# Optimization experiments

Measured on AMD Instinct MI355X. Metric: run time of the kernel, lower is better.

The kernel has to match this reference:

```python
import jax, jax.numpy as jnp
import numpy as np
import math

EMBED_DIM = 64

def setup_inputs() -> dict:
    key = jax.random.key(0)
    ks = jax.random.split(key, 9)
    B, S, H, E = 2, 2048, 8, EMBED_DIM
    f16 = jnp.float16
    inp = {
        'query': jax.random.normal(ks[0], (B, S, H, E), dtype=f16),
        'key':   jax.random.normal(ks[1], (B, S, H, E), dtype=f16),
        'value': jax.random.normal(ks[2], (B, S, H, E), dtype=f16),
        # Linear params (torch Linear: y = x @ W.T + b); W stored as [out,in]
        'Wq': (jax.random.normal(ks[3], (E, E), dtype=f16) / np.float16(math.sqrt(E))),
        'bq': jax.random.normal(ks[4], (E,), dtype=f16) * np.float16(0.02),
        'Wk': (jax.random.normal(ks[5], (E, E), dtype=f16) / np.float16(math.sqrt(E))),
        'bk': jax.random.normal(ks[6], (E,), dtype=f16) * np.float16(0.02),
        'Wv': (jax.random.normal(ks[7], (E, E), dtype=f16) / np.float16(math.sqrt(E))),
        'bv': jax.random.normal(ks[8], (E,), dtype=f16) * np.float16(0.02),
    }
    return inp

def reference(query, key, value, Wq, bq, Wk, bk, Wv, bv):
    # Linear projections on last dim, fused with permute(0,2,1,3): [B,S,H,E] -> [B,H,S,E]
    q = jnp.einsum('bshe,fe->bhsf', query, Wq) + bq
    k = jnp.einsum('bshe,fe->bhsf', key, Wk) + bk
    v = jnp.einsum('bshe,fe->bhsf', value, Wv) + bv
    scale = jnp.asarray(1.0 / math.sqrt(q.shape[-1]), dtype=q.dtype)
    q = q * scale
    # full attention matrix [B,H,S,S], fp16 matmul then fp32 softmax (faithful to source)
    scores = jnp.einsum('bhse,bhte->bhst', q, k).astype(jnp.float32)
    attn = jax.nn.softmax(scores, axis=-1).astype(jnp.float16)
    out = jnp.einsum('bhst,bhte->bhse', attn, v)
    return out
```

## Files before the change

### kernel.cpp

```cpp
#include <hip/hip_runtime.h>

#define S_LEN 2048
#define NH    8
#define EMB   64
#define BM    64
#define BN    64
#define NKT   (S_LEN / BN)
#define NSPLIT 2
#define M_INIT  (-1.0e4f)
#define EXP_CLAMP (-80.0f)
#define DEFER_THR 8.0f

typedef _Float16 half8   __attribute__((ext_vector_type(8)));
typedef _Float16 half4   __attribute__((ext_vector_type(4)));
typedef float    float4_t __attribute__((ext_vector_type(4)));
typedef float    float8_t __attribute__((ext_vector_type(8)));

__device__ inline half8 cvt8(const float* p) {
    float8_t f = *reinterpret_cast<const float8_t*>(p);
    half8 h;
    #pragma unroll
    for (int j = 0; j < 8; ++j) h[j] = (_Float16)f[j];
    return h;
}

__device__ inline void gload_lds16(const _Float16* g, _Float16* l) {
    __builtin_amdgcn_global_load_lds(
        (const __attribute__((address_space(1))) void*)g,
        (__attribute__((address_space(3))) void*)l, 16, 0, 0);
}

__device__ inline void proj_body(
    int mode, int bid, const float* __restrict__ X,
    const float* __restrict__ W, const float* __restrict__ bias,
    _Float16* __restrict__ Dst)
{
    const int tid  = threadIdx.x;
    const int lane = tid & 63;
    const int wave = tid >> 6;
    const int l15  = lane & 15;
    const int quad = lane >> 4;
    const int gwave = bid * 4 + wave;

    half8 wf[4][2];
    #pragma unroll
    for (int ft = 0; ft < 4; ++ft)
        #pragma unroll
        for (int ks = 0; ks < 2; ++ks)
            wf[ft][ks] = cvt8(W + (ft * 16 + l15) * 64 + ks * 32 + quad * 8);
    float bv[4];
    #pragma unroll
    for (int ft = 0; ft < 4; ++ft) bv[ft] = bias[ft * 16 + l15];

    #pragma unroll
    for (int rt2 = 0; rt2 < 2; ++rt2) {
        const int rt = gwave * 2 + rt2;
        const int arow = rt * 16 + l15;
        half8 xf[2];
        #pragma unroll
        for (int ks = 0; ks < 2; ++ks)
            xf[ks] = cvt8(X + (long)arow * 64 + ks * 32 + quad * 8);
        float4_t acc[4];
        #pragma unroll
        for (int ft = 0; ft < 4; ++ft) {
            acc[ft] = (float4_t){0.f, 0.f, 0.f, 0.f};
            #pragma unroll
            for (int ks = 0; ks < 2; ++ks)
                acc[ft] = __builtin_amdgcn_mfma_f32_16x16x32_f16(
                    xf[ks], wf[ft][ks], acc[ft], 0, 0, 0);
        }
        #pragma unroll
        for (int r = 0; r < 4; ++r) {
            const int row = rt * 16 + quad * 4 + r;
            const int b = row >> 14;
            const int s = (row >> 3) & 2047;
            const int h = row & 7;
            const int bh = b * NH + h;
            #pragma unroll
            for (int ft = 0; ft < 4; ++ft) {
                const _Float16 v = (_Float16)(acc[ft][r] + bv[ft]);
                const int f = ft * 16 + l15;
                if (mode == 0)
                    Dst[((long)bh * S_LEN + s) * EMB + f] = v * (_Float16)0.125f;
                else if (mode == 1)
                    Dst[(((long)bh * 8 + (f >> 3)) * S_LEN + s) * 8 + (f & 7)] = v;
                else
                    Dst[(((long)bh * 256 + (s >> 3)) * 64 + f) * 8 + (s & 7)] = v;
            }
        }
    }
}

__global__ __launch_bounds__(256) void proj_qk(
    const float* __restrict__ q_in, const float* __restrict__ k_in,
    const float* __restrict__ Wq, const float* __restrict__ bq,
    const float* __restrict__ Wk, const float* __restrict__ bk,
    _Float16* __restrict__ Qf16, _Float16* __restrict__ KT8)
{
    const int seg = blockIdx.x >> 8;
    const int bid = blockIdx.x & 255;
    if (seg == 0) proj_body(0, bid, q_in, Wq, bq, Qf16);
    else          proj_body(1, bid, k_in, Wk, bk, KT8);
}

__global__ __launch_bounds__(256) void proj_v(
    const float* __restrict__ v_in,
    const float* __restrict__ Wv, const float* __restrict__ bv_,
    _Float16* __restrict__ VT8)
{
    proj_body(2, blockIdx.x, v_in, Wv, bv_, VT8);
}

__global__ __launch_bounds__(256, 4) void attn_part(
    const _Float16* __restrict__ KT, const _Float16* __restrict__ VT,
    const _Float16* __restrict__ Qf16,
    _Float16* __restrict__ p0, _Float16* __restrict__ p1,
    float* __restrict__ stats)
{
    __shared__ __align__(16) _Float16 Kb[2][8 * 64 * 8];
    __shared__ __align__(16) _Float16 Vb[2][8 * 64 * 8];
    __shared__ __align__(16) _Float16 Pl[4][16 * 64];

    const int tid  = threadIdx.x;
    const int lane = tid & 63;
    const int wave = tid >> 6;
    const int l15  = lane & 15;
    const int quad = lane >> 4;

    const int bx     = blockIdx.x;
    const int xcd    = bx & 7;
    const int j      = bx >> 3;
    const int hh     = j >> 6;
    const int within = j & 63;
    const int bh     = xcd * 2 + hh;
    const int qt     = within >> 1;
    const int sp     = within & 1;

    const int qrow0 = qt * BM + wave * 16;
    const _Float16* kg  = KT + (long)bh * 8 * S_LEN * 8;
    const _Float16* vgh = VT + (long)bh * 256 * 512;

    const _Float16* k0 = kg + ((long)(tid >> 6) * S_LEN + (tid & 63)) * 8;
    const _Float16* k1 = kg + ((long)((tid >> 6) + 4) * S_LEN + (tid & 63)) * 8;
    const _Float16* v0 = vgh + tid * 8;
    const _Float16* v1 = vgh + (256 + tid) * 8;

    const int kb = sp * (NKT / NSPLIT), ke = kb + (NKT / NSPLIT);

    {
        const long t8  = (long)(kb * BN) * 8;
        const long t64 = (long)(kb * BN) * 64;
        gload_lds16(k0 + t8,  &Kb[0][tid * 8]);
        gload_lds16(k1 + t8,  &Kb[0][(256 + tid) * 8]);
        gload_lds16(v0 + t64, &Vb[0][tid * 8]);
        gload_lds16(v1 + t64, &Vb[0][(256 + tid) * 8]);
    }

    half8 qf[2];
    {
        const _Float16* qrow = Qf16 + ((long)bh * S_LEN + qrow0 + l15) * EMB;
        qf[0] = *reinterpret_cast<const half8*>(qrow + quad * 8);
        qf[1] = *reinterpret_cast<const half8*>(qrow + 32 + quad * 8);
    }

    half8 vones;
    #pragma unroll
    for (int jj = 0; jj < 8; ++jj) vones[jj] = (_Float16)1.0f;

    float4_t o[4];
    #pragma unroll
    for (int et = 0; et < 4; ++et) o[et] = (float4_t){0.f, 0.f, 0.f, 0.f};
    float4_t lacc = (float4_t){0.f, 0.f, 0.f, 0.f};
    float m_run = M_INIT;

    const int pswz = (l15 & 7) << 3;
    _Float16* Pw = Pl[wave];

    __syncthreads();

    for (int kt = kb; kt < ke; ++kt) {
        const int cur = (kt - kb) & 1;
        const bool more = (kt + 1 < ke);

        if (more) {
            const long t8  = (long)((kt + 1) * BN) * 8;
            const long t64 = (long)((kt + 1) * BN) * 64;
            _Float16* kd = Kb[cur ^ 1];
            _Float16* vd = Vb[cur ^ 1];
            gload_lds16(k0 + t8,  kd + tid * 8);
            gload_lds16(k1 + t8,  kd + (256 + tid) * 8);
            gload_lds16(v0 + t64, vd + tid * 8);
            gload_lds16(v1 + t64, vd + (256 + tid) * 8);
        }

        const _Float16* Kc = Kb[cur];
        const _Float16* Vc = Vb[cur];

        float4_t sacc[4];
        #pragma unroll
        for (int nt = 0; nt < 4; ++nt) sacc[nt] = (float4_t){0.f, 0.f, 0.f, 0.f};
        __builtin_amdgcn_s_setprio(1);
        #pragma unroll
        for (int nt = 0; nt < 4; ++nt)
            #pragma unroll
            for (int ks = 0; ks < 2; ++ks) {
                half8 kf = *reinterpret_cast<const half8*>(
                    Kc + (ks * 4 + quad) * 512 + (nt * 16 + l15) * 8);
                sacc[nt] = __builtin_amdgcn_mfma_f32_16x16x32_f16(
                    kf, qf[ks], sacc[nt], 0, 0, 0);
            }
        __builtin_amdgcn_s_setprio(0);

        float mx = fmaxf(fmaxf(sacc[0][0], sacc[0][1]),
                         fmaxf(sacc[0][2], sacc[0][3]));
        mx = fmaxf(fmaxf(mx, sacc[1][0]), sacc[1][1]);
        mx = fmaxf(fmaxf(mx, sacc[1][2]), sacc[1][3]);
        mx = fmaxf(fmaxf(mx, sacc[2][0]), sacc[2][1]);
        mx = fmaxf(fmaxf(mx, sacc[2][2]), sacc[2][3]);
        mx = fmaxf(fmaxf(mx, sacc[3][0]), sacc[3][1]);
        mx = fmaxf(fmaxf(mx, sacc[3][2]), sacc[3][3]);

        if (!__all(mx - m_run <= DEFER_THR)) {
            float mr = fmaxf(mx, __shfl_xor(mx, 16));
            mr = fmaxf(mr, __shfl_xor(mr, 32));
            const float mn = fmaxf(m_run, mr);
            const float alpha = __expf(fmaxf(m_run - mn, EXP_CLAMP));
            m_run = mn;
            #pragma unroll
            for (int r = 0; r < 4; ++r) {
                const float ar = __shfl(alpha, quad * 4 + r);
                lacc[r] *= ar;
                #pragma unroll
                for (int et = 0; et < 4; ++et) o[et][r] *= ar;
            }
        }

        #pragma unroll
        for (int ts = 0; ts < 2; ++ts) {
            #pragma unroll
            for (int ntl = 0; ntl < 2; ++ntl) {
                const int nt = ts * 2 + ntl;
                half4 ph;
                #pragma unroll
                for (int r = 0; r < 4; ++r)
                    ph[r] = (_Float16)__expf(sacc[nt][r] - m_run);
                *reinterpret_cast<half4*>(
                    &Pw[l15 * 64 + ((nt * 16 + quad * 4) ^ pswz)]) = ph;
            }
            half8 pf = *reinterpret_cast<const half8*>(
                &Pw[l15 * 64 + ((ts * 32 + quad * 8) ^ pswz)]);
            __builtin_amdgcn_s_setprio(1);
            #pragma unroll
            for (int et = 0; et < 4; ++et) {
                half8 vf = *reinterpret_cast<const half8*>(
                    Vc + (ts * 4 + quad) * 512 + (et * 16 + l15) * 8);
                o[et] = __builtin_amdgcn_mfma_f32_16x16x32_f16(pf, vf, o[et], 0, 0, 0);
            }
            lacc = __builtin_amdgcn_mfma_f32_16x16x32_f16(pf, vones, lacc, 0, 0, 0);
            __builtin_amdgcn_s_setprio(0);
        }

        if (more) __syncthreads();
    }

    _Float16* pp = (sp == 0) ? p0 : p1;
    #pragma unroll
    for (int r = 0; r < 4; ++r) {
        const float inv = 1.f / lacc[r];
        const int row = qrow0 + quad * 4 + r;
        const int R = bh * S_LEN + row;
        #pragma unroll
        for (int et = 0; et < 4; ++et)
            pp[(long)R * EMB + et * 16 + l15] = (_Float16)(o[et][r] * inv);
    }
    {
        const int srcl = (lane >> 2) * 16;
        const float s0 = __shfl(lacc[0], srcl);
        const float s1 = __shfl(lacc[1], srcl);
        const float s2 = __shfl(lacc[2], srcl);
        const float s3 = __shfl(lacc[3], srcl);
        const int rr = lane & 3;
        const float lsel = (rr == 0) ? s0 : (rr == 1) ? s1 : (rr == 2) ? s2 : s3;
        if (lane < 16) {
            const int R = bh * S_LEN + qrow0 + lane;
            stats[sp * 32768 + R] = m_run;
            stats[(NSPLIT + sp) * 32768 + R] = lsel;
        }
    }
}

__global__ __launch_bounds__(256) void attn_combine(
    const _Float16* __restrict__ p0, const _Float16* __restrict__ p1,
    const float* __restrict__ stats, float* __restrict__ out)
{
    const int gid = blockIdx.x * 256 + threadIdx.x;
    const int R  = gid >> 2;
    const int c0 = (gid & 3) * 16;
    const float m0 = stats[R], m1 = stats[32768 + R];
    const float l0 = stats[2 * 32768 + R], l1 = stats[3 * 32768 + R];
    const float M = fmaxf(m0, m1);
    float w0 = l0 * __expf(fmaxf(m0 - M, EXP_CLAMP));
    float w1 = l1 * __expf(fmaxf(m1 - M, EXP_CLAMP));
    const float rinv = 1.f / (w0 + w1);
    w0 *= rinv; w1 *= rinv;
    const long i0 = (long)R * EMB + c0;
    #pragma unroll
    for (int h = 0; h < 2; ++h) {
        half8 a = *reinterpret_cast<const half8*>(p0 + i0 + h * 8);
        half8 b = *reinterpret_cast<const half8*>(p1 + i0 + h * 8);
        #pragma unroll
        for (int j = 0; j < 8; ++j)
            out[i0 + h * 8 + j] = (float)(_Float16)(
                w0 * (float)a[j] + w1 * (float)b[j]);
    }
}

extern "C" void kernel_launch(void* const* d_in, const int* in_sizes, int n_in,
                              void* d_out, int out_size, void* d_ws, size_t ws_size,
                              hipStream_t stream) {
    const float* q_in = (const float*)d_in[0];
    const float* k_in = (const float*)d_in[1];
    const float* v_in = (const float*)d_in[2];
    const float* Wq   = (const float*)d_in[3];
    const float* bq   = (const float*)d_in[4];
    const float* Wk   = (const float*)d_in[5];
    const float* bk   = (const float*)d_in[6];
    const float* Wv   = (const float*)d_in[7];
    const float* bv   = (const float*)d_in[8];
    float* out = (float*)d_out;

    _Float16* Qf16  = (_Float16*)d_out;
    _Float16* KT8   = (_Float16*)((char*)d_out + (4u << 20));
    _Float16* VT8   = (_Float16*)d_in[1];
    _Float16* part0 = (_Float16*)d_in[2];
    _Float16* part1 = part0 + (long)2 * 1024 * 1024;
    float*    stats = (float*)d_in[0];

    proj_qk<<<512, 256, 0, stream>>>(q_in, k_in, Wq, bq, Wk, bk, Qf16, KT8);
    proj_v<<<256, 256, 0, stream>>>(v_in, Wv, bv, VT8);
    attn_part<<<16 * 32 * NSPLIT, 256, 0, stream>>>(KT8, VT8, Qf16,
                                                    part0, part1, stats);
    attn_combine<<<512, 256, 0, stream>>>(part0, part1, stats, out);
}
```

Measured before the change: 137.5 us.

## Split KV into three parts and software-pipeline QK^T one tile ahead

Raises the key-sequence split from two to three, so more blocks are launched (1536), and the combine kernel merges three partial outputs. It also restructures the main loop: the QK^T MFMAs for the next tile are issued before softmax and PV of the current tile, with K double-buffered and V triple-buffered in LDS, two tiles prefetched ahead. The goal is to overlap matrix work with exp and LDS latency and to fill more CUs. In exchange it uses more registers and LDS (occupancy hint drops to 3), adds another partial buffer to write and read, and stores the partials and stats in input buffers.

```diff
diff --git a/kernel.cpp b/kernel.cpp
--- a/kernel.cpp
+++ b/kernel.cpp
@@ -6,7 +6,7 @@
 #define BM    64
 #define BN    64
 #define NKT   (S_LEN / BN)
-#define NSPLIT 2
+#define NSPLIT 3
 #define M_INIT  (-1.0e4f)
 #define EXP_CLAMP (-80.0f)
 #define DEFER_THR 8.0f
@@ -111,14 +111,14 @@
     proj_body(2, blockIdx.x, v_in, Wv, bv_, VT8);
 }
 
-__global__ __launch_bounds__(256, 4) void attn_part(
+__global__ __launch_bounds__(256, 3) void attn_part(
     const _Float16* __restrict__ KT, const _Float16* __restrict__ VT,
     const _Float16* __restrict__ Qf16,
     _Float16* __restrict__ p0, _Float16* __restrict__ p1,
-    float* __restrict__ stats)
+    _Float16* __restrict__ p2, float* __restrict__ stats)
 {
     __shared__ __align__(16) _Float16 Kb[2][8 * 64 * 8];
-    __shared__ __align__(16) _Float16 Vb[2][8 * 64 * 8];
+    __shared__ __align__(16) _Float16 Vb[3][8 * 64 * 8];
     __shared__ __align__(16) _Float16 Pl[4][16 * 64];
 
     const int tid  = threadIdx.x;
@@ -130,11 +130,11 @@
     const int bx     = blockIdx.x;
     const int xcd    = bx & 7;
     const int j      = bx >> 3;
-    const int hh     = j >> 6;
-    const int within = j & 63;
+    const int hh     = (j >= 96) ? 1 : 0;
+    const int within = j - hh * 96;
     const int bh     = xcd * 2 + hh;
-    const int qt     = within >> 1;
-    const int sp     = within & 1;
+    const int qt     = within / NSPLIT;
+    const int sp     = within - qt * NSPLIT;
 
     const int qrow0 = qt * BM + wave * 16;
     const _Float16* kg  = KT + (long)bh * 8 * S_LEN * 8;
@@ -145,7 +145,8 @@
     const _Float16* v0 = vgh + tid * 8;
     const _Float16* v1 = vgh + (256 + tid) * 8;
 
-    const int kb = sp * (NKT / NSPLIT), ke = kb + (NKT / NSPLIT);
+    const int kb = (sp * NKT) / NSPLIT, ke = ((sp + 1) * NKT) / NSPLIT;
+    const int ntile = ke - kb;
 
     {
         const long t8  = (long)(kb * BN) * 8;
@@ -155,6 +156,14 @@
         gload_lds16(v0 + t64, &Vb[0][tid * 8]);
         gload_lds16(v1 + t64, &Vb[0][(256 + tid) * 8]);
     }
+    {
+        const long t8  = (long)((kb + 1) * BN) * 8;
+        const long t64 = (long)((kb + 1) * BN) * 64;
+        gload_lds16(k0 + t8,  &Kb[1][tid * 8]);
+        gload_lds16(k1 + t8,  &Kb[1][(256 + tid) * 8]);
+        gload_lds16(v0 + t64, &Vb[1][tid * 8]);
+        gload_lds16(v1 + t64, &Vb[1][(256 + tid) * 8]);
+    }
 
     half8 qf[2];
     {
@@ -178,47 +187,63 @@
 
     __syncthreads();
 
-    for (int kt = kb; kt < ke; ++kt) {
-        const int cur = (kt - kb) & 1;
-        const bool more = (kt + 1 < ke);
-
-        if (more) {
-            const long t8  = (long)((kt + 1) * BN) * 8;
-            const long t64 = (long)((kt + 1) * BN) * 64;
-            _Float16* kd = Kb[cur ^ 1];
-            _Float16* vd = Vb[cur ^ 1];
+    float4_t cur[4];
+    #pragma unroll
+    for (int nt = 0; nt < 4; ++nt) cur[nt] = (float4_t){0.f, 0.f, 0.f, 0.f};
+    __builtin_amdgcn_s_setprio(1);
+    #pragma unroll
+    for (int nt = 0; nt < 4; ++nt)
+        #pragma unroll
+        for (int ks = 0; ks < 2; ++ks) {
+            half8 kf = *reinterpret_cast<const half8*>(
+                &Kb[0][(ks * 4 + quad) * 512 + (nt * 16 + l15) * 8]);
+            cur[nt] = __builtin_amdgcn_mfma_f32_16x16x32_f16(
+                kf, qf[ks], cur[nt], 0, 0, 0);
+        }
+    __builtin_amdgcn_s_setprio(0);
+    __syncthreads();
+
+    int vs_stage = 2;
+    int vs_pv    = 0;
+
+    for (int it = 0; it < ntile; ++it) {
+        if (it + 2 < ntile) {
+            const long t8  = (long)((kb + it + 2) * BN) * 8;
+            const long t64 = (long)((kb + it + 2) * BN) * 64;
+            _Float16* kd = Kb[it & 1];
+            _Float16* vd = Vb[vs_stage];
             gload_lds16(k0 + t8,  kd + tid * 8);
             gload_lds16(k1 + t8,  kd + (256 + tid) * 8);
             gload_lds16(v0 + t64, vd + tid * 8);
             gload_lds16(v1 + t64, vd + (256 + tid) * 8);
         }
 
-        const _Float16* Kc = Kb[cur];
-        const _Float16* Vc = Vb[cur];
-
-        float4_t sacc[4];
-        #pragma unroll
-        for (int nt = 0; nt < 4; ++nt) sacc[nt] = (float4_t){0.f, 0.f, 0.f, 0.f};
-        __builtin_amdgcn_s_setprio(1);
-        #pragma unroll
-        for (int nt = 0; nt < 4; ++nt)
-            #pragma unroll
-            for (int ks = 0; ks < 2; ++ks) {
-                half8 kf = *reinterpret_cast<const half8*>(
-                    Kc + (ks * 4 + quad) * 512 + (nt * 16 + l15) * 8);
-                sacc[nt] = __builtin_amdgcn_mfma_f32_16x16x32_f16(
-                    kf, qf[ks], sacc[nt], 0, 0, 0);
-            }
-        __builtin_amdgcn_s_setprio(0);
-
-        float mx = fmaxf(fmaxf(sacc[0][0], sacc[0][1]),
-                         fmaxf(sacc[0][2], sacc[0][3]));
-        mx = fmaxf(fmaxf(mx, sacc[1][0]), sacc[1][1]);
-        mx = fmaxf(fmaxf(mx, sacc[1][2]), sacc[1][3]);
-        mx = fmaxf(fmaxf(mx, sacc[2][0]), sacc[2][1]);
-        mx = fmaxf(fmaxf(mx, sacc[2][2]), sacc[2][3]);
-        mx = fmaxf(fmaxf(mx, sacc[3][0]), sacc[3][1]);
-        mx = fmaxf(fmaxf(mx, sacc[3][2]), sacc[3][3]);
+        float4_t nxt[4];
+        #pragma unroll
+        for (int nt = 0; nt < 4; ++nt) nxt[nt] = (float4_t){0.f, 0.f, 0.f, 0.f};
+        if (it + 1 < ntile) {
+            const _Float16* Kc = Kb[(it + 1) & 1];
+            __builtin_amdgcn_s_setprio(1);
+            #pragma unroll
+            for (int nt = 0; nt < 4; ++nt)
+                #pragma unroll
+                for (int ks = 0; ks < 2; ++ks) {
+                    half8 kf = *reinterpret_cast<const half8*>(
+                        Kc + (ks * 4 + quad) * 512 + (nt * 16 + l15) * 8);
+                    nxt[nt] = __builtin_amdgcn_mfma_f32_16x16x32_f16(
+                        kf, qf[ks], nxt[nt], 0, 0, 0);
+                }
+            __builtin_amdgcn_s_setprio(0);
+        }
+
+        float mx = fmaxf(fmaxf(cur[0][0], cur[0][1]),
+                         fmaxf(cur[0][2], cur[0][3]));
+        mx = fmaxf(fmaxf(mx, cur[1][0]), cur[1][1]);
+        mx = fmaxf(fmaxf(mx, cur[1][2]), cur[1][3]);
+        mx = fmaxf(fmaxf(mx, cur[2][0]), cur[2][1]);
+        mx = fmaxf(fmaxf(mx, cur[2][2]), cur[2][3]);
+        mx = fmaxf(fmaxf(mx, cur[3][0]), cur[3][1]);
+        mx = fmaxf(fmaxf(mx, cur[3][2]), cur[3][3]);
 
         if (!__all(mx - m_run <= DEFER_THR)) {
             float mr = fmaxf(mx, __shfl_xor(mx, 16));
@@ -235,6 +260,7 @@
             }
         }
 
+        const _Float16* Vc = Vb[vs_pv];
         #pragma unroll
         for (int ts = 0; ts < 2; ++ts) {
             #pragma unroll
@@ -243,7 +269,7 @@
                 half4 ph;
                 #pragma unroll
                 for (int r = 0; r < 4; ++r)
-                    ph[r] = (_Float16)__expf(sacc[nt][r] - m_run);
+                    ph[r] = (_Float16)__expf(cur[nt][r] - m_run);
                 *reinterpret_cast<half4*>(
                     &Pw[l15 * 64 + ((nt * 16 + quad * 4) ^ pswz)]) = ph;
             }
@@ -260,10 +286,15 @@
             __builtin_amdgcn_s_setprio(0);
         }
 
-        if (more) __syncthreads();
-    }
-
-    _Float16* pp = (sp == 0) ? p0 : p1;
+        if (it + 1 < ntile) __syncthreads();
+
+        #pragma unroll
+        for (int nt = 0; nt < 4; ++nt) cur[nt] = nxt[nt];
+        vs_pv    = (vs_pv == 2)    ? 0 : vs_pv + 1;
+        vs_stage = (vs_stage == 2) ? 0 : vs_stage + 1;
+    }
+
+    _Float16* pp = (sp == 0) ? p0 : (sp == 1) ? p1 : p2;
     #pragma unroll
     for (int r = 0; r < 4; ++r) {
         const float inv = 1.f / lacc[r];
@@ -291,27 +322,31 @@
 
 __global__ __launch_bounds__(256) void attn_combine(
     const _Float16* __restrict__ p0, const _Float16* __restrict__ p1,
-    const float* __restrict__ stats, float* __restrict__ out)
+    const _Float16* __restrict__ p2, const float* __restrict__ stats,
+    float* __restrict__ out)
 {
     const int gid = blockIdx.x * 256 + threadIdx.x;
     const int R  = gid >> 2;
     const int c0 = (gid & 3) * 16;
-    const float m0 = stats[R], m1 = stats[32768 + R];
-    const float l0 = stats[2 * 32768 + R], l1 = stats[3 * 32768 + R];
-    const float M = fmaxf(m0, m1);
+    const float m0 = stats[R], m1 = stats[32768 + R], m2 = stats[2 * 32768 + R];
+    const float l0 = stats[3 * 32768 + R], l1 = stats[4 * 32768 + R],
+                l2 = stats[5 * 32768 + R];
+    const float M = fmaxf(fmaxf(m0, m1), m2);
     float w0 = l0 * __expf(fmaxf(m0 - M, EXP_CLAMP));
     float w1 = l1 * __expf(fmaxf(m1 - M, EXP_CLAMP));
-    const float rinv = 1.f / (w0 + w1);
-    w0 *= rinv; w1 *= rinv;
+    float w2 = l2 * __expf(fmaxf(m2 - M, EXP_CLAMP));
+    const float rinv = 1.f / (w0 + w1 + w2);
+    w0 *= rinv; w1 *= rinv; w2 *= rinv;
     const long i0 = (long)R * EMB + c0;
     #pragma unroll
     for (int h = 0; h < 2; ++h) {
         half8 a = *reinterpret_cast<const half8*>(p0 + i0 + h * 8);
         half8 b = *reinterpret_cast<const half8*>(p1 + i0 + h * 8);
+        half8 c = *reinterpret_cast<const half8*>(p2 + i0 + h * 8);
         #pragma unroll
         for (int j = 0; j < 8; ++j)
             out[i0 + h * 8 + j] = (float)(_Float16)(
-                w0 * (float)a[j] + w1 * (float)b[j]);
+                w0 * (float)a[j] + w1 * (float)b[j] + w2 * (float)c[j]);
     }
 }
 
@@ -334,11 +369,12 @@
     _Float16* VT8   = (_Float16*)d_in[1];
     _Float16* part0 = (_Float16*)d_in[2];
     _Float16* part1 = part0 + (long)2 * 1024 * 1024;
-    float*    stats = (float*)d_in[0];
+    _Float16* part2 = (_Float16*)d_in[0];
+    float*    stats = (float*)((char*)d_in[0] + (4u << 20));
 
     proj_qk<<<512, 256, 0, stream>>>(q_in, k_in, Wq, bq, Wk, bk, Qf16, KT8);
     proj_v<<<256, 256, 0, stream>>>(v_in, Wv, bv, VT8);
     attn_part<<<16 * 32 * NSPLIT, 256, 0, stream>>>(KT8, VT8, Qf16,
-                                                    part0, part1, stats);
-    attn_combine<<<512, 256, 0, stream>>>(part0, part1, stats, out);
-}
+                                                    part0, part1, part2, stats);
+    attn_combine<<<512, 256, 0, stream>>>(part0, part1, part2, stats, out);
+}
```

After: 139.5 us. Within noise of the previous version (+1.5%).
